# Kernel tuning notes

Measured on AMD Instinct MI355X. Metric: run time of the kernel, lower is better.

## Reference

```python
import jax, jax.numpy as jnp
import numpy as np

B, IN, OUT, NW = 8192, 4096, 4096, 16
NH, ND2 = NW // 3, NW // 3          # 5 haar, 5 db2
ND4 = NW - NH - ND2                  # 6 db4

DB2_HI = jnp.array([-0.1294095225512604, -0.2241438680420134,
                    0.8365163037378079, -0.4829629131445341], dtype=jnp.float32)
DB4_HI = jnp.array([-0.0074578275060427, -0.0233534968567756, 0.0218081502370024,
                    0.1323683939878645, -0.0197721859913265, -0.4461007108737368,
                    0.5055922216746659, -0.1629171572809054], dtype=jnp.float32)


def setup_inputs() -> dict:
    key = jax.random.key(0)
    ks = jax.random.split(key, 4)
    x = jax.random.normal(ks[0], (B, IN), dtype=jnp.float32)
    # kaiming-normal fan_in linear init -> std = 1/sqrt(fan_in); biases zero
    lin_w = jax.random.normal(ks[1], (OUT, IN), dtype=jnp.float32) * (1.0 / np.sqrt(IN))
    lin_b = jnp.zeros((OUT,), jnp.float32)
    proj_w = jax.random.normal(ks[2], (NW, IN), dtype=jnp.float32) * (1.0 / np.sqrt(IN))
    proj_b = jnp.zeros((NW,), jnp.float32)
    # exact _init_parameters values for the 'mixed' case
    scales = jnp.concatenate([jnp.logspace(-0.5, 0.5, NH),
                              jnp.logspace(-0.3, 0.7, ND2),
                              jnp.logspace(-0.3, 0.7, ND4)]).astype(jnp.float32)
    translations = jnp.concatenate([jnp.linspace(-1.5, 1.5, NH),
                                    jnp.linspace(-1.5, 1.5, ND2),
                                    jnp.linspace(-1.5, 1.5, ND4)]).astype(jnp.float32)
    comb_w = jax.random.normal(ks[3], (OUT, NW), dtype=jnp.float32) * (1.0 / np.sqrt(NW))
    comb_b = jnp.zeros((OUT,), jnp.float32)
    ln_g = jnp.ones((OUT,), jnp.float32)
    ln_beta = jnp.zeros((OUT,), jnp.float32)
    return dict(x=x, lin_w=lin_w, lin_b=lin_b, proj_w=proj_w, proj_b=proj_b,
                scales=scales, translations=translations,
                comb_w=comb_w, comb_b=comb_b, ln_g=ln_g, ln_beta=ln_beta)


def _haar_mother(sx):
    # Haar mother wavelet: +1 on [0, 0.5), -1 on [0.5, 1)
    return (((sx >= 0.0) & (sx < 0.5)).astype(jnp.float32)
            - ((sx >= 0.5) & (sx < 1.0)).astype(jnp.float32))


def _db_feature(val, scale, trans, filt, max_shift, mult):
    # db*_wavelet_transform + simplified_transform (scalar per wavelet)
    scale_factor = jax.nn.sigmoid(scale) * 2.0
    shift = jnp.clip(jnp.round(trans * mult), 0, max_shift).astype(jnp.int32)
    f = jnp.roll(filt, shift) * scale_factor
    feat = jnp.mean(val * jnp.sin(f * 5.0))
    return feat / (jnp.sum(jnp.abs(f)) * 0.1)  # filter_sum always > 0 here


def reference(x, lin_w, lin_b, proj_w, proj_b, scales, translations,
              comb_w, comb_b, ln_g, ln_beta):
    direct = x @ lin_w.T + lin_b                 # [B, OUT]
    proj = x @ proj_w.T + proj_b                 # [B, NW]

    # Haar wavelets on first NH projected channels (elementwise, per batch)
    sx = (proj[:, :NH] - translations[:NH]) / scales[:NH]
    haar = _haar_mother(sx)                      # [B, NH]

    # Daubechies 'simplified_transform': mean of first min(4,B) batch entries per column
    vals = jnp.mean(proj[:4, :], axis=0)         # [NW]
    db2 = jax.vmap(lambda v, s, t: _db_feature(v, s, t, DB2_HI, 3, 4.0))(
        vals[NH:NH + ND2], scales[NH:NH + ND2], translations[NH:NH + ND2])
    db4 = jax.vmap(lambda v, s, t: _db_feature(v, s, t, DB4_HI, 7, 8.0))(
        vals[NH + ND2:], scales[NH + ND2:], translations[NH + ND2:])
    db = jnp.broadcast_to(jnp.concatenate([db2, db4])[None, :],
                          (x.shape[0], ND2 + ND4))  # [B, ND2+ND4]

    wave = jnp.concatenate([haar, db], axis=1)   # [B, NW]
    wave_path = wave @ comb_w.T + comb_b         # [B, OUT]

    y = direct + wave_path
    mu = jnp.mean(y, axis=-1, keepdims=True)
    var = jnp.mean((y - mu) ** 2, axis=-1, keepdims=True)
    return (y - mu) * jax.lax.rsqrt(var + 1e-5) * ln_g + ln_beta
```

## Files before the change

kernel.cpp:

```cpp
#include <hip/hip_runtime.h>
#include <hip/hip_bf16.h>
#include <stdint.h>

constexpr int BDIM = 8192;
constexpr int INDIM = 4096;
constexpr int OUTDIM = 4096;

typedef __attribute__((ext_vector_type(8))) short bf16x8;
typedef __attribute__((ext_vector_type(8))) short short8;
typedef __attribute__((ext_vector_type(4))) float f32x4;

__device__ __forceinline__ uint16_t f2bf_rne(float f) {
  union { float f; uint32_t u; } v; v.f = f;
  uint32_t r = v.u + 0x7fffu + ((v.u >> 16) & 1u);
  return (uint16_t)(r >> 16);
}
__device__ __forceinline__ float bf2f(uint16_t h) {
  union { uint32_t u; float f; } v; v.u = ((uint32_t)h) << 16; return v.f;
}

__device__ __forceinline__ void gload_lds16(const void* g, void* l) {
  __builtin_amdgcn_global_load_lds(
      (const __attribute__((address_space(1))) void*)g,
      (__attribute__((address_space(3))) void*)l, 16, 0, 0);
}

__global__ __launch_bounds__(256) void k_pre(
    const float* __restrict__ x, const float* __restrict__ lin_w,
    const float* __restrict__ proj_w, const float* __restrict__ proj_b,
    const float* __restrict__ scales, const float* __restrict__ trans,
    const float* __restrict__ lin_b, const float* __restrict__ comb_w,
    const float* __restrict__ comb_b, uint16_t* __restrict__ xb,
    uint16_t* __restrict__ wb, float* __restrict__ haar,
    float* __restrict__ cvec, float* __restrict__ W5) {
  const int tid = threadIdx.x;
  const int lane = tid & 63, w = tid >> 6;

  if (blockIdx.x < 8192) {
    const int row = blockIdx.x;
    const float4* xr = (const float4*)(x + (size_t)row * INDIM);
    short8* xbr = (short8*)(xb + (size_t)row * INDIM);
    float acc[5] = {0.f, 0.f, 0.f, 0.f, 0.f};
#pragma unroll
    for (int c = 0; c < 2; ++c) {
      int i8 = tid + c * 256;
      float4 v0 = xr[i8 * 2];
      float4 v1 = xr[i8 * 2 + 1];
      short8 o;
      o[0] = (short)f2bf_rne(v0.x); o[1] = (short)f2bf_rne(v0.y);
      o[2] = (short)f2bf_rne(v0.z); o[3] = (short)f2bf_rne(v0.w);
      o[4] = (short)f2bf_rne(v1.x); o[5] = (short)f2bf_rne(v1.y);
      o[6] = (short)f2bf_rne(v1.z); o[7] = (short)f2bf_rne(v1.w);
      xbr[i8] = o;
#pragma unroll
      for (int j = 0; j < 5; ++j) {
        const float4* pj = (const float4*)(proj_w + (size_t)j * INDIM);
        float4 p0 = pj[i8 * 2];
        float4 p1 = pj[i8 * 2 + 1];
        acc[j] += v0.x * p0.x + v0.y * p0.y + v0.z * p0.z + v0.w * p0.w;
        acc[j] += v1.x * p1.x + v1.y * p1.y + v1.z * p1.z + v1.w * p1.w;
      }
    }
    __shared__ float wred[4][5];
#pragma unroll
    for (int j = 0; j < 5; ++j) {
      float v = acc[j];
#pragma unroll
      for (int off = 32; off; off >>= 1) v += __shfl_down(v, off, 64);
      if (lane == 0) wred[w][j] = v;
    }
    __syncthreads();
    if (tid < 5) {
      float p = wred[0][tid] + wred[1][tid] + wred[2][tid] + wred[3][tid]
                + proj_b[tid];
      float sx = (p - trans[tid]) / scales[tid];
      float h = 0.f;
      if (sx >= 0.f && sx < 0.5f) h = 1.f;
      else if (sx >= 0.5f && sx < 1.f) h = -1.f;
      haar[(size_t)row * 5 + tid] = h;
    }
  } else if (blockIdx.x < 10240) {
    const int bid = blockIdx.x - 8192;
    const int n8 = (OUTDIM * INDIM) / 8;
    const float4* w4 = (const float4*)lin_w;
    short8* wb8 = (short8*)wb;
    for (int i = bid * 256 + tid; i < n8; i += 2048 * 256) {
      float4 v0 = w4[i * 2];
      float4 v1 = w4[i * 2 + 1];
      short8 o;
      o[0] = (short)f2bf_rne(v0.x); o[1] = (short)f2bf_rne(v0.y);
      o[2] = (short)f2bf_rne(v0.z); o[3] = (short)f2bf_rne(v0.w);
      o[4] = (short)f2bf_rne(v1.x); o[5] = (short)f2bf_rne(v1.y);
      o[6] = (short)f2bf_rne(v1.z); o[7] = (short)f2bf_rne(v1.w);
      wb8[i] = o;
    }
  } else {
    __shared__ float wred[4][11];
    __shared__ float dbs[11];
    float acc[11];
#pragma unroll
    for (int j = 0; j < 11; ++j) acc[j] = 0.f;
    for (int r = 0; r < 4; ++r) {
      const float4* xr = (const float4*)(x + (size_t)r * INDIM);
      for (int c = tid; c < INDIM / 4; c += 256) {
        float4 v = xr[c];
#pragma unroll
        for (int j = 0; j < 11; ++j) {
          float4 p = ((const float4*)(proj_w + (size_t)(j + 5) * INDIM))[c];
          acc[j] += v.x * p.x + v.y * p.y + v.z * p.z + v.w * p.w;
        }
      }
    }
#pragma unroll
    for (int j = 0; j < 11; ++j) {
      float v = acc[j];
#pragma unroll
      for (int off = 32; off; off >>= 1) v += __shfl_down(v, off, 64);
      if (lane == 0) wred[w][j] = v;
    }
    __syncthreads();
    if (tid == 0) {
      const float DB2[4] = {-0.1294095225512604f, -0.2241438680420134f,
                            0.8365163037378079f, -0.4829629131445341f};
      const float DB4[8] = {-0.0074578275060427f, -0.0233534968567756f,
                            0.0218081502370024f,  0.1323683939878645f,
                            -0.0197721859913265f, -0.4461007108737368f,
                            0.5055922216746659f,  -0.1629171572809054f};
      for (int j = 0; j < 11; ++j) {
        float sum = wred[0][j] + wred[1][j] + wred[2][j] + wred[3][j];
        float val = sum * 0.25f + proj_b[j + 5];
        float sc = scales[j + 5];
        float sf = 2.f / (1.f + expf(-sc));
        const float* filt = (j < 5) ? DB2 : DB4;
        int L = (j < 5) ? 4 : 8;
        float ssin = 0.f, sabs = 0.f;
        for (int i = 0; i < L; ++i) {
          float fi = filt[i] * sf;
          ssin += sinf(fi * 5.0f);
          sabs += fabsf(fi);
        }
        dbs[j] = val * (ssin / (float)L) / (sabs * 0.1f);
      }
    }
    __syncthreads();
    for (int o = tid; o < OUTDIM; o += 256) {
      const float* cw = comb_w + (size_t)o * 16;
      float cc = lin_b[o] + comb_b[o];
#pragma unroll
      for (int j = 0; j < 11; ++j) cc += dbs[j] * cw[5 + j];
      cvec[o] = cc;
#pragma unroll
      for (int j = 0; j < 5; ++j) W5[j * OUTDIM + o] = cw[j];
    }
  }
}


#define BARX() __builtin_amdgcn_s_barrier()
#define LGKM0() do { asm volatile("s_waitcnt lgkmcnt(0)" ::: "memory"); \
                     __builtin_amdgcn_sched_barrier(0); } while (0)
#define VM6() asm volatile("s_waitcnt vmcnt(6)" ::: "memory")

#define STAGE_A(t, q) do { \
  const char* _s = aSrc + (size_t)(q) * 64 * 8192 + (size_t)((t) & 63) * 128; \
  char* _l = sA + ((t) & 1) * 32768 + (q) * 8192 + ldsStage; \
  gload_lds16(_s, _l); gload_lds16(_s + 128 * 8192, _l + 16384); } while (0)

#define STAGE_B(t, h) do { \
  const char* _s = bSrc + (size_t)(h) * 128 * 8192 + (size_t)((t) & 63) * 128; \
  char* _l = sB + ((t) & 1) * 32768 + (h) * 16384 + ldsStage; \
  gload_lds16(_s, _l); gload_lds16(_s + 64 * 8192, _l + 8192); } while (0)

#define RDA4(buf, mb) do { const char* _p = sA + (buf) * 32768; \
  _Pragma("unroll") for (int _m = 0; _m < 4; ++_m) { \
    ar[_m][0] = *(const bf16x8*)(_p + (aoff + ((mb) + _m) * 2048)); \
    ar[_m][1] = *(const bf16x8*)(_p + ((aoff ^ 64) + ((mb) + _m) * 2048)); } } while (0)

#define RDB2(buf, arr, nb) do { const char* _p = sB + (buf) * 32768; \
  _Pragma("unroll") for (int _n = 0; _n < 2; ++_n) { \
    arr[_n][0] = *(const bf16x8*)(_p + (boff + ((nb) + _n) * 2048)); \
    arr[_n][1] = *(const bf16x8*)(_p + ((boff ^ 64) + ((nb) + _n) * 2048)); } } while (0)

#define MF8(mb, arrB, nb) do { \
  __builtin_amdgcn_s_setprio(1); \
  _Pragma("unroll") for (int _m = 0; _m < 4; ++_m) \
  _Pragma("unroll") for (int _n = 0; _n < 2; ++_n) { \
    acc[(mb) + _m][(nb) + _n] = __builtin_amdgcn_mfma_f32_16x16x32_bf16( \
        ar[_m][0], arrB[_n][0], acc[(mb) + _m][(nb) + _n], 0, 0, 0); \
    acc[(mb) + _m][(nb) + _n] = __builtin_amdgcn_mfma_f32_16x16x32_bf16( \
        ar[_m][1], arrB[_n][1], acc[(mb) + _m][(nb) + _n], 0, 0, 0); } \
  __builtin_amdgcn_s_setprio(0); } while (0)

template <bool WB>
__global__ __launch_bounds__(512, 2) void k_gemm(const uint16_t* __restrict__ A,
                                                 const uint16_t* __restrict__ Bw,
                                                 float* __restrict__ C,
                                                 uint16_t* __restrict__ Ybf) {
  constexpr int K = INDIM;
  constexpr int N = OUTDIM;
  extern __shared__ char smem[];
  char* sA = smem;
  char* sB = smem + 65536;

  const int tid = threadIdx.x;
  const int wid = tid >> 6;
  const int lane = tid & 63;
  const int l15 = lane & 15;
  const int kh = lane >> 4;
  const int wm = wid >> 2;
  const int wn = wid & 3;

  const int nwg = gridDim.x;
  const int bid = blockIdx.x;
  const int wg = (bid & 7) * (nwg >> 3) + (bid >> 3);
  constexpr int NBN = N / 256;
  const int mblk = wg / NBN, nblk = wg % NBN;
  const size_t arow = (size_t)mblk * 256, brow = (size_t)nblk * 256;

  const int srow = tid >> 3;
  const int scol = ((tid & 7) * 16) ^ ((srow & 7) << 4);
  const char* aSrc = (const char*)A + (arow + srow) * 8192 + scol;
  const char* bSrc = (const char*)Bw + (brow + srow) * 8192 + scol;
  const int ldsStage = wid * 1024;

  const int col0 = (kh * 16) ^ ((l15 & 7) << 4);
  const int aoff = (wm * 128 + l15) * 128 + col0;
  const int boff = (wn * 64 + l15) * 128 + col0;

  f32x4 acc[8][4];
#pragma unroll
  for (int m = 0; m < 8; ++m)
#pragma unroll
    for (int n = 0; n < 4; ++n) acc[m][n] = (f32x4){0.f, 0.f, 0.f, 0.f};
  bf16x8 ar[4][2], b01[2][2], b23[2][2];

  STAGE_A(0, 0); STAGE_A(0, 1); STAGE_B(0, 0); STAGE_B(0, 1);
  STAGE_A(1, 0); STAGE_B(1, 0); STAGE_B(1, 1);
  VM6(); BARX();

  for (int it = 0; it < K / 128; ++it) {
    const int t1 = it * 2 + 1, t2 = it * 2 + 2, t3 = it * 2 + 3;
    RDA4(0, 0); RDB2(0, b01, 0);
    STAGE_A(t1, 1);
    BARX(); LGKM0(); MF8(0, b01, 0); BARX();
    RDB2(0, b23, 2);
    STAGE_A(t2, 0);
    BARX(); LGKM0(); MF8(0, b23, 2); BARX();
    RDA4(0, 4);
    STAGE_B(t2, 0);
    BARX(); LGKM0(); MF8(4, b01, 0); BARX();
    STAGE_B(t2, 1);
    BARX(); LGKM0(); MF8(4, b23, 2);
    VM6(); BARX();
    RDA4(1, 0); RDB2(1, b01, 0);
    STAGE_A(t2, 1);
    BARX(); LGKM0(); MF8(0, b01, 0); BARX();
    RDB2(1, b23, 2);
    STAGE_A(t3, 0);
    BARX(); LGKM0(); MF8(0, b23, 2); BARX();
    RDA4(1, 4);
    STAGE_B(t3, 0);
    BARX(); LGKM0(); MF8(4, b01, 0); BARX();
    STAGE_B(t3, 1);
    BARX(); LGKM0(); MF8(4, b23, 2);
    VM6(); BARX();
  }

  const size_t crow0 = arow + (size_t)wm * 128;
  const int ccol0 = (int)brow + wn * 64;
#pragma unroll
  for (int m = 0; m < 8; ++m) {
#pragma unroll
    for (int n = 0; n < 4; ++n) {
      if constexpr (WB) {
        uint16_t* yp = Ybf + (crow0 + m * 16 + kh * 4) * (size_t)N
                       + ccol0 + n * 16 + l15;
#pragma unroll
        for (int j = 0; j < 4; ++j) yp[(size_t)j * N] = f2bf_rne(acc[m][n][j]);
      } else {
        float* cp = C + (crow0 + m * 16 + kh * 4) * N + ccol0 + n * 16 + l15;
#pragma unroll
        for (int j = 0; j < 4; ++j) cp[(size_t)j * N] = acc[m][n][j];
      }
    }
  }
}

template <bool RB>
__global__ __launch_bounds__(256) void k_ln(
    float* __restrict__ out, const uint16_t* __restrict__ ybf,
    const float* __restrict__ haar, const float* __restrict__ cvec,
    const float* __restrict__ W5, const float* __restrict__ g,
    const float* __restrict__ beta) {
  const int row = blockIdx.x;
  const int tid = threadIdx.x;
  const float h0 = haar[(size_t)row * 5 + 0];
  const float h1 = haar[(size_t)row * 5 + 1];
  const float h2 = haar[(size_t)row * 5 + 2];
  const float h3 = haar[(size_t)row * 5 + 3];
  const float h4 = haar[(size_t)row * 5 + 4];
  float* yrow = out + (size_t)row * OUTDIM;
  const ushort4* ybr = (const ushort4*)(ybf + (size_t)row * OUTDIM);
  const float4* yfr = (const float4*)yrow;

  float4 vals[4];
  float s = 0.f, s2 = 0.f;
#pragma unroll
  for (int c = 0; c < 4; ++c) {
    int i4 = tid + c * 256;
    float4 d;
    if constexpr (RB) {
      ushort4 u = ybr[i4];
      d.x = bf2f(u.x); d.y = bf2f(u.y); d.z = bf2f(u.z); d.w = bf2f(u.w);
    } else {
      d = yfr[i4];
    }
    float4 cv = ((const float4*)cvec)[i4];
    float4 w0 = ((const float4*)(W5 + 0 * OUTDIM))[i4];
    float4 w1 = ((const float4*)(W5 + 1 * OUTDIM))[i4];
    float4 w2 = ((const float4*)(W5 + 2 * OUTDIM))[i4];
    float4 w3 = ((const float4*)(W5 + 3 * OUTDIM))[i4];
    float4 w4 = ((const float4*)(W5 + 4 * OUTDIM))[i4];
    float4 t;
    t.x = d.x + cv.x + h0 * w0.x + h1 * w1.x + h2 * w2.x + h3 * w3.x + h4 * w4.x;
    t.y = d.y + cv.y + h0 * w0.y + h1 * w1.y + h2 * w2.y + h3 * w3.y + h4 * w4.y;
    t.z = d.z + cv.z + h0 * w0.z + h1 * w1.z + h2 * w2.z + h3 * w3.z + h4 * w4.z;
    t.w = d.w + cv.w + h0 * w0.w + h1 * w1.w + h2 * w2.w + h3 * w3.w + h4 * w4.w;
    vals[c] = t;
    s += t.x + t.y + t.z + t.w;
    s2 += t.x * t.x + t.y * t.y + t.z * t.z + t.w * t.w;
  }

  const int lane = tid & 63, w = tid >> 6;
#pragma unroll
  for (int off = 32; off; off >>= 1) {
    s += __shfl_down(s, off, 64);
    s2 += __shfl_down(s2, off, 64);
  }
  __shared__ float rs[4], rs2[4];
  __shared__ float smu, sinv;
  if (lane == 0) { rs[w] = s; rs2[w] = s2; }
  __syncthreads();
  if (tid == 0) {
    float S = rs[0] + rs[1] + rs[2] + rs[3];
    float S2 = rs2[0] + rs2[1] + rs2[2] + rs2[3];
    float mu = S / (float)OUTDIM;
    float var = S2 / (float)OUTDIM - mu * mu;
    smu = mu;
    sinv = rsqrtf(var + 1e-5f);
  }
  __syncthreads();
  const float mu = smu, inv = sinv;
  float4* yo = (float4*)yrow;
#pragma unroll
  for (int c = 0; c < 4; ++c) {
    int i4 = tid + c * 256;
    float4 gg = ((const float4*)g)[i4];
    float4 bb = ((const float4*)beta)[i4];
    float4 t = vals[c];
    float4 o;
    o.x = (t.x - mu) * inv * gg.x + bb.x;
    o.y = (t.y - mu) * inv * gg.y + bb.y;
    o.z = (t.z - mu) * inv * gg.z + bb.z;
    o.w = (t.w - mu) * inv * gg.w + bb.w;
    yo[i4] = o;
  }
}

extern "C" void kernel_launch(void* const* d_in, const int* in_sizes, int n_in,
                              void* d_out, int out_size, void* d_ws, size_t ws_size,
                              hipStream_t stream) {
  const float* x      = (const float*)d_in[0];
  const float* lin_w  = (const float*)d_in[1];
  const float* lin_b  = (const float*)d_in[2];
  const float* proj_w = (const float*)d_in[3];
  const float* proj_b = (const float*)d_in[4];
  const float* scales = (const float*)d_in[5];
  const float* trans  = (const float*)d_in[6];
  const float* comb_w = (const float*)d_in[7];
  const float* comb_b = (const float*)d_in[8];
  const float* ln_g   = (const float*)d_in[9];
  const float* ln_b   = (const float*)d_in[10];
  float* out = (float*)d_out;

  char* ws = (char*)d_ws;
  uint16_t* xb   = (uint16_t*)ws;
  uint16_t* wb   = (uint16_t*)(ws + 67108864);
  float*    haar = (float*)(ws + 100663296);
  float*    cvec = (float*)(ws + 100827136);
  float*    W5   = (float*)(ws + 100843520);
  uint16_t* ybf  = (uint16_t*)(ws + 100925440);
  const bool bf16y = ws_size >= 168034304ull;

  hipFuncSetAttribute((const void*)k_gemm<true>,
                      hipFuncAttributeMaxDynamicSharedMemorySize, 131072);
  hipFuncSetAttribute((const void*)k_gemm<false>,
                      hipFuncAttributeMaxDynamicSharedMemorySize, 131072);

  k_pre<<<10241, 256, 0, stream>>>(x, lin_w, proj_w, proj_b, scales, trans,
                                   lin_b, comb_w, comb_b, xb, wb, haar, cvec, W5);
  if (bf16y) {
    k_gemm<true><<<(BDIM / 256) * (OUTDIM / 256), 512, 131072, stream>>>(
        xb, wb, out, ybf);
    k_ln<true><<<BDIM, 256, 0, stream>>>(out, ybf, haar, cvec, W5, ln_g, ln_b);
  } else {
    k_gemm<false><<<(BDIM / 256) * (OUTDIM / 256), 512, 131072, stream>>>(
        xb, wb, out, ybf);
    k_ln<false><<<BDIM, 256, 0, stream>>>(out, ybf, haar, cvec, W5, ln_g, ln_b);
  }
}
```

Measured before the change: 380.6 us.

## Cache proj_w and W5 in LDS, process 16 rows per block with wave-per-row

The prologue kernel now stages the five Haar projection rows in shared memory and has each wave handle four rows, cutting 8192 blocks down to 512. The LayerNorm kernel likewise stages the five W5 rows in LDS and uses one wave per row, 16 rows per block, with a pure wave-level xor reduction instead of block syncs. This removes repeated global/L2 reads of the shared weight vectors and the per-row block barriers. In exchange, 80KB of static LDS limits occupancy, and the 64-register float4 row buffer raises register pressure. Fewer blocks also means less parallelism to hide memory latency.

```diff
diff --git a/kernel.cpp b/kernel.cpp
--- a/kernel.cpp
+++ b/kernel.cpp
@@ -33,58 +33,58 @@
     const float* __restrict__ comb_b, uint16_t* __restrict__ xb,
     uint16_t* __restrict__ wb, float* __restrict__ haar,
     float* __restrict__ cvec, float* __restrict__ W5) {
+  __shared__ float pj[5 * 4096];
   const int tid = threadIdx.x;
   const int lane = tid & 63, w = tid >> 6;
 
-  if (blockIdx.x < 8192) {
-    const int row = blockIdx.x;
-    const float4* xr = (const float4*)(x + (size_t)row * INDIM);
-    short8* xbr = (short8*)(xb + (size_t)row * INDIM);
-    float acc[5] = {0.f, 0.f, 0.f, 0.f, 0.f};
-#pragma unroll
-    for (int c = 0; c < 2; ++c) {
-      int i8 = tid + c * 256;
-      float4 v0 = xr[i8 * 2];
-      float4 v1 = xr[i8 * 2 + 1];
-      short8 o;
-      o[0] = (short)f2bf_rne(v0.x); o[1] = (short)f2bf_rne(v0.y);
-      o[2] = (short)f2bf_rne(v0.z); o[3] = (short)f2bf_rne(v0.w);
-      o[4] = (short)f2bf_rne(v1.x); o[5] = (short)f2bf_rne(v1.y);
-      o[6] = (short)f2bf_rne(v1.z); o[7] = (short)f2bf_rne(v1.w);
-      xbr[i8] = o;
+  if (blockIdx.x < 512) {
+    float4* pj4 = (float4*)pj;
+    const float4* pw4 = (const float4*)proj_w;
+    for (int i = tid; i < 5 * 1024; i += 256) pj4[i] = pw4[i];
+    __syncthreads();
+    const int row0 = blockIdx.x * 16 + w * 4;
+    for (int rr = 0; rr < 4; ++rr) {
+      const int row = row0 + rr;
+      const float4* xr = (const float4*)(x + (size_t)row * INDIM);
+      ushort4* xbr = (ushort4*)(xb + (size_t)row * INDIM);
+      float a[5] = {0.f, 0.f, 0.f, 0.f, 0.f};
+#pragma unroll
+      for (int k = 0; k < 16; ++k) {
+        int i4 = lane + k * 64;
+        float4 v = xr[i4];
+        ushort4 o;
+        o.x = f2bf_rne(v.x); o.y = f2bf_rne(v.y);
+        o.z = f2bf_rne(v.z); o.w = f2bf_rne(v.w);
+        xbr[i4] = o;
+#pragma unroll
+        for (int j = 0; j < 5; ++j) {
+          float4 p = pj4[j * 1024 + i4];
+          a[j] += v.x * p.x + v.y * p.y + v.z * p.z + v.w * p.w;
+        }
+      }
 #pragma unroll
       for (int j = 0; j < 5; ++j) {
-        const float4* pj = (const float4*)(proj_w + (size_t)j * INDIM);
-        float4 p0 = pj[i8 * 2];
-        float4 p1 = pj[i8 * 2 + 1];
-        acc[j] += v0.x * p0.x + v0.y * p0.y + v0.z * p0.z + v0.w * p0.w;
-        acc[j] += v1.x * p1.x + v1.y * p1.y + v1.z * p1.z + v1.w * p1.w;
-      }
-    }
-    __shared__ float wred[4][5];
-#pragma unroll
-    for (int j = 0; j < 5; ++j) {
-      float v = acc[j];
-#pragma unroll
-      for (int off = 32; off; off >>= 1) v += __shfl_down(v, off, 64);
-      if (lane == 0) wred[w][j] = v;
-    }
-    __syncthreads();
-    if (tid < 5) {
-      float p = wred[0][tid] + wred[1][tid] + wred[2][tid] + wred[3][tid]
-                + proj_b[tid];
-      float sx = (p - trans[tid]) / scales[tid];
-      float h = 0.f;
-      if (sx >= 0.f && sx < 0.5f) h = 1.f;
-      else if (sx >= 0.5f && sx < 1.f) h = -1.f;
-      haar[(size_t)row * 5 + tid] = h;
-    }
-  } else if (blockIdx.x < 10240) {
-    const int bid = blockIdx.x - 8192;
+#pragma unroll
+        for (int off = 32; off; off >>= 1) a[j] += __shfl_down(a[j], off, 64);
+      }
+      if (lane == 0) {
+#pragma unroll
+        for (int j = 0; j < 5; ++j) {
+          float p = a[j] + proj_b[j];
+          float sx = (p - trans[j]) / scales[j];
+          float h = 0.f;
+          if (sx >= 0.f && sx < 0.5f) h = 1.f;
+          else if (sx >= 0.5f && sx < 1.f) h = -1.f;
+          haar[(size_t)row * 5 + j] = h;
+        }
+      }
+    }
+  } else if (blockIdx.x < 1024) {
+    const int bid = blockIdx.x - 512;
     const int n8 = (OUTDIM * INDIM) / 8;
     const float4* w4 = (const float4*)lin_w;
     short8* wb8 = (short8*)wb;
-    for (int i = bid * 256 + tid; i < n8; i += 2048 * 256) {
+    for (int i = bid * 256 + tid; i < n8; i += 512 * 256) {
       float4 v0 = w4[i * 2];
       float4 v1 = w4[i * 2 + 1];
       short8 o;
@@ -95,8 +95,8 @@
       wb8[i] = o;
     }
   } else {
-    __shared__ float wred[4][11];
-    __shared__ float dbs[11];
+    float* wred = pj;
+    float* dbs = pj + 64;
     float acc[11];
 #pragma unroll
     for (int j = 0; j < 11; ++j) acc[j] = 0.f;
@@ -116,7 +116,7 @@
       float v = acc[j];
 #pragma unroll
       for (int off = 32; off; off >>= 1) v += __shfl_down(v, off, 64);
-      if (lane == 0) wred[w][j] = v;
+      if (lane == 0) wred[w * 11 + j] = v;
     }
     __syncthreads();
     if (tid == 0) {
@@ -127,7 +127,8 @@
                             -0.0197721859913265f, -0.4461007108737368f,
                             0.5055922216746659f,  -0.1629171572809054f};
       for (int j = 0; j < 11; ++j) {
-        float sum = wred[0][j] + wred[1][j] + wred[2][j] + wred[3][j];
+        float sum = wred[0 * 11 + j] + wred[1 * 11 + j] + wred[2 * 11 + j] +
+                    wred[3 * 11 + j];
         float val = sum * 0.25f + proj_b[j + 5];
         float sc = scales[j + 5];
         float sf = 2.f / (1.f + expf(-sc));
@@ -292,78 +293,72 @@
     const float* __restrict__ haar, const float* __restrict__ cvec,
     const float* __restrict__ W5, const float* __restrict__ g,
     const float* __restrict__ beta) {
-  const int row = blockIdx.x;
-  const int tid = threadIdx.x;
-  const float h0 = haar[(size_t)row * 5 + 0];
-  const float h1 = haar[(size_t)row * 5 + 1];
-  const float h2 = haar[(size_t)row * 5 + 2];
-  const float h3 = haar[(size_t)row * 5 + 3];
-  const float h4 = haar[(size_t)row * 5 + 4];
-  float* yrow = out + (size_t)row * OUTDIM;
-  const ushort4* ybr = (const ushort4*)(ybf + (size_t)row * OUTDIM);
-  const float4* yfr = (const float4*)yrow;
-
-  float4 vals[4];
-  float s = 0.f, s2 = 0.f;
-#pragma unroll
-  for (int c = 0; c < 4; ++c) {
-    int i4 = tid + c * 256;
-    float4 d;
-    if constexpr (RB) {
-      ushort4 u = ybr[i4];
-      d.x = bf2f(u.x); d.y = bf2f(u.y); d.z = bf2f(u.z); d.w = bf2f(u.w);
-    } else {
-      d = yfr[i4];
-    }
-    float4 cv = ((const float4*)cvec)[i4];
-    float4 w0 = ((const float4*)(W5 + 0 * OUTDIM))[i4];
-    float4 w1 = ((const float4*)(W5 + 1 * OUTDIM))[i4];
-    float4 w2 = ((const float4*)(W5 + 2 * OUTDIM))[i4];
-    float4 w3 = ((const float4*)(W5 + 3 * OUTDIM))[i4];
-    float4 w4 = ((const float4*)(W5 + 4 * OUTDIM))[i4];
-    float4 t;
-    t.x = d.x + cv.x + h0 * w0.x + h1 * w1.x + h2 * w2.x + h3 * w3.x + h4 * w4.x;
-    t.y = d.y + cv.y + h0 * w0.y + h1 * w1.y + h2 * w2.y + h3 * w3.y + h4 * w4.y;
-    t.z = d.z + cv.z + h0 * w0.z + h1 * w1.z + h2 * w2.z + h3 * w3.z + h4 * w4.z;
-    t.w = d.w + cv.w + h0 * w0.w + h1 * w1.w + h2 * w2.w + h3 * w3.w + h4 * w4.w;
-    vals[c] = t;
-    s += t.x + t.y + t.z + t.w;
-    s2 += t.x * t.x + t.y * t.y + t.z * t.z + t.w * t.w;
-  }
-
-  const int lane = tid & 63, w = tid >> 6;
-#pragma unroll
-  for (int off = 32; off; off >>= 1) {
-    s += __shfl_down(s, off, 64);
-    s2 += __shfl_down(s2, off, 64);
-  }
-  __shared__ float rs[4], rs2[4];
-  __shared__ float smu, sinv;
-  if (lane == 0) { rs[w] = s; rs2[w] = s2; }
+  __shared__ float w5l[5 * 4096];
+  const int tid = threadIdx.x, lane = tid & 63, w = tid >> 6;
+  float4* w54 = (float4*)w5l;
+  const float4* W54 = (const float4*)W5;
+  for (int i = tid; i < 5 * 1024; i += 256) w54[i] = W54[i];
   __syncthreads();
-  if (tid == 0) {
-    float S = rs[0] + rs[1] + rs[2] + rs[3];
-    float S2 = rs2[0] + rs2[1] + rs2[2] + rs2[3];
-    float mu = S / (float)OUTDIM;
-    float var = S2 / (float)OUTDIM - mu * mu;
-    smu = mu;
-    sinv = rsqrtf(var + 1e-5f);
-  }
-  __syncthreads();
-  const float mu = smu, inv = sinv;
-  float4* yo = (float4*)yrow;
-#pragma unroll
-  for (int c = 0; c < 4; ++c) {
-    int i4 = tid + c * 256;
-    float4 gg = ((const float4*)g)[i4];
-    float4 bb = ((const float4*)beta)[i4];
-    float4 t = vals[c];
-    float4 o;
-    o.x = (t.x - mu) * inv * gg.x + bb.x;
-    o.y = (t.y - mu) * inv * gg.y + bb.y;
-    o.z = (t.z - mu) * inv * gg.z + bb.z;
-    o.w = (t.w - mu) * inv * gg.w + bb.w;
-    yo[i4] = o;
+
+  const int row0 = blockIdx.x * 16 + w * 4;
+  for (int rr = 0; rr < 4; ++rr) {
+    const int row = row0 + rr;
+    const float h0 = haar[(size_t)row * 5 + 0];
+    const float h1 = haar[(size_t)row * 5 + 1];
+    const float h2 = haar[(size_t)row * 5 + 2];
+    const float h3 = haar[(size_t)row * 5 + 3];
+    const float h4 = haar[(size_t)row * 5 + 4];
+    const ushort4* ybr = (const ushort4*)(ybf + (size_t)row * OUTDIM);
+    const float4* yfr = (const float4*)(out + (size_t)row * OUTDIM);
+
+    float4 vals[16];
+    float s = 0.f, s2 = 0.f;
+#pragma unroll
+    for (int k = 0; k < 16; ++k) {
+      int i4 = lane + k * 64;
+      float4 d;
+      if constexpr (RB) {
+        ushort4 u = ybr[i4];
+        d.x = bf2f(u.x); d.y = bf2f(u.y); d.z = bf2f(u.z); d.w = bf2f(u.w);
+      } else {
+        d = yfr[i4];
+      }
+      float4 cv = ((const float4*)cvec)[i4];
+      float4 w0 = w54[0 * 1024 + i4];
+      float4 w1 = w54[1 * 1024 + i4];
+      float4 w2 = w54[2 * 1024 + i4];
+      float4 w3 = w54[3 * 1024 + i4];
+      float4 w4 = w54[4 * 1024 + i4];
+      float4 t;
+      t.x = d.x + cv.x + h0 * w0.x + h1 * w1.x + h2 * w2.x + h3 * w3.x + h4 * w4.x;
+      t.y = d.y + cv.y + h0 * w0.y + h1 * w1.y + h2 * w2.y + h3 * w3.y + h4 * w4.y;
+      t.z = d.z + cv.z + h0 * w0.z + h1 * w1.z + h2 * w2.z + h3 * w3.z + h4 * w4.z;
+      t.w = d.w + cv.w + h0 * w0.w + h1 * w1.w + h2 * w2.w + h3 * w3.w + h4 * w4.w;
+      vals[k] = t;
+      s += t.x + t.y + t.z + t.w;
+      s2 += t.x * t.x + t.y * t.y + t.z * t.z + t.w * t.w;
+    }
+#pragma unroll
+    for (int off = 32; off; off >>= 1) {
+      s += __shfl_xor(s, off, 64);
+      s2 += __shfl_xor(s2, off, 64);
+    }
+    const float mu = s / (float)OUTDIM;
+    const float inv = rsqrtf(s2 / (float)OUTDIM - mu * mu + 1e-5f);
+    float4* yo = (float4*)(out + (size_t)row * OUTDIM);
+#pragma unroll
+    for (int k = 0; k < 16; ++k) {
+      int i4 = lane + k * 64;
+      float4 gg = ((const float4*)g)[i4];
+      float4 bb = ((const float4*)beta)[i4];
+      float4 t = vals[k];
+      float4 o;
+      o.x = (t.x - mu) * inv * gg.x + bb.x;
+      o.y = (t.y - mu) * inv * gg.y + bb.y;
+      o.z = (t.z - mu) * inv * gg.z + bb.z;
+      o.w = (t.w - mu) * inv * gg.w + bb.w;
+      yo[i4] = o;
+    }
   }
 }
 
@@ -397,15 +392,15 @@
   hipFuncSetAttribute((const void*)k_gemm<false>,
                       hipFuncAttributeMaxDynamicSharedMemorySize, 131072);
 
-  k_pre<<<10241, 256, 0, stream>>>(x, lin_w, proj_w, proj_b, scales, trans,
-                                   lin_b, comb_w, comb_b, xb, wb, haar, cvec, W5);
+  k_pre<<<1025, 256, 0, stream>>>(x, lin_w, proj_w, proj_b, scales, trans,
+                                  lin_b, comb_w, comb_b, xb, wb, haar, cvec, W5);
   if (bf16y) {
     k_gemm<true><<<(BDIM / 256) * (OUTDIM / 256), 512, 131072, stream>>>(
         xb, wb, out, ybf);
-    k_ln<true><<<BDIM, 256, 0, stream>>>(out, ybf, haar, cvec, W5, ln_g, ln_b);
+    k_ln<true><<<BDIM / 16, 256, 0, stream>>>(out, ybf, haar, cvec, W5, ln_g, ln_b);
   } else {
     k_gemm<false><<<(BDIM / 256) * (OUTDIM / 256), 512, 131072, stream>>>(
         xb, wb, out, ybf);
-    k_ln<false><<<BDIM, 256, 0, stream>>>(out, ybf, haar, cvec, W5, ln_g, ln_b);
+    k_ln<false><<<BDIM / 16, 256, 0, stream>>>(out, ybf, haar, cvec, W5, ln_g, ln_b);
   }
 }
```

Result: slower. 495.4 us (+30.2%).
